# Performance work log

Hardware: AMD Instinct MI355X
Metric: run time of the kernel (lower is better)

## Reference

```python
import jax, jax.numpy as jnp
import numpy as np

B, N, C, H, W_, K, POS = 1, 100000, 128, 256, 256, 4, 36


def setup_inputs() -> dict:
    key = jax.random.key(0)
    ks = jax.random.split(key, 12)
    inp = {}
    # query coords in [-1, 1] (grid_sample normalized space)
    inp["query"] = jax.random.uniform(ks[0], (B, N, 3), jnp.float32, -1.0, 1.0)
    inp["pe"] = jax.random.normal(ks[1], (B, N, POS), jnp.float32)
    for i, p in enumerate(["xy", "xz", "yz"]):
        inp[f"feat_{p}"] = jax.random.normal(ks[2 + i], (B, C, H, W_), jnp.float32)
        inp[f"Wa_{p}"] = jax.random.normal(ks[5 + i], (POS, K), jnp.float32) * 0.1
        inp[f"ba_{p}"] = jnp.zeros((K,), jnp.float32)
        # offsets initialized to zero in the module; use small random so sampling is non-trivial
        inp[f"Wo_{p}"] = jax.random.normal(ks[8 + i], (POS, 2 * K), jnp.float32) * 0.02
        inp[f"bo_{p}"] = jnp.zeros((2 * K,), jnp.float32)
    return inp


def _bilinear_border(feat, gx, gy):
    """F.grid_sample(feat, grid, align_corners=False, padding_mode='border').
    feat: [B,C,H,W]; gx,gy: [B,N,K] normalized x (width) and y (height) coords.
    Returns [B,C,N,K]."""
    b, c, h, w = feat.shape
    # unnormalize (align_corners=False) then border-clip
    x = jnp.clip(((gx + 1.0) * w - 1.0) * 0.5, 0.0, w - 1.0)
    y = jnp.clip(((gy + 1.0) * h - 1.0) * 0.5, 0.0, h - 1.0)
    x0 = jnp.floor(x)
    y0 = jnp.floor(y)
    wx = x - x0  # [B,N,K]
    wy = y - y0
    xi0 = x0.astype(jnp.int32)
    yi0 = y0.astype(jnp.int32)
    xi1 = jnp.minimum(xi0 + 1, w - 1)
    yi1 = jnp.minimum(yi0 + 1, h - 1)
    ff = feat.reshape(b, c, h * w)
    gather = jax.vmap(lambda f, lin: f[:, lin])  # [C,HW],[N,K] -> [C,N,K]
    v00 = gather(ff, yi0 * w + xi0)
    v01 = gather(ff, yi0 * w + xi1)
    v10 = gather(ff, yi1 * w + xi0)
    v11 = gather(ff, yi1 * w + xi1)
    wx_ = wx[:, None]
    wy_ = wy[:, None]
    return (v00 * (1.0 - wx_) * (1.0 - wy_) + v01 * wx_ * (1.0 - wy_)
            + v10 * (1.0 - wx_) * wy_ + v11 * wx_ * wy_)


def _sample_plane(coords, pe, feat, Wa, ba, Wo, bo):
    b, n, _ = coords.shape
    attn = jax.nn.softmax(pe @ Wa + ba, axis=-1)            # [B,N,K]
    off = (pe @ Wo + bo).reshape(b, n, K, 2)                 # [B,N,K,2]
    sc = coords[:, :, None, :] + off                         # [B,N,K,2]
    # torch code flips last dim before grid_sample: grid x = sc[...,1], y = sc[...,0]
    sampled = _bilinear_border(feat, sc[..., 1], sc[..., 0])  # [B,C,N,K]
    out = jnp.einsum('bcnk,bnk->bnc', sampled, attn)         # weighted sum over K
    return out


def reference(query, pe, feat_xy, feat_xz, feat_yz,
              Wa_xy, ba_xy, Wo_xy, bo_xy,
              Wa_xz, ba_xz, Wo_xz, bo_xz,
              Wa_yz, ba_yz, Wo_yz, bo_yz):
    idx_xy = jnp.array([0, 1])
    idx_xz = jnp.array([0, 2])
    idx_yz = jnp.array([1, 2])
    f_xy = _sample_plane(query[..., idx_xy], pe, feat_xy, Wa_xy, ba_xy, Wo_xy, bo_xy)
    f_xz = _sample_plane(query[..., idx_xz], pe, feat_xz, Wa_xz, ba_xz, Wo_xz, bo_xz)
    f_yz = _sample_plane(query[..., idx_yz], pe, feat_yz, Wa_yz, ba_yz, Wo_yz, bo_yz)
    return f_xy + f_xz + f_yz
```

## Files before the change

### kernel.cpp

```cpp
#include <hip/hip_runtime.h>
#include <hip/hip_fp16.h>
#include <math.h>

#define NQ   100000
#define CCH  128
#define HDIM 256
#define WDIM 256
#define HW   (HDIM * WDIM)
#define KPTS 4
#define PDIM 36
#define NBIN 32768
#define RECW 40

#define WBLK ((NQ + 255) / 256)
#define TBLK ((HW / 64) * (CCH / 64) * 3)

__device__ inline int axis_bin(float x) {
  int b = (int)((x + 1.0f) * 16.0f);
  return min(31, max(0, b));
}
__device__ inline unsigned int spread5(unsigned int x) {
  return (x & 1u) | ((x & 2u) << 2) | ((x & 4u) << 4) | ((x & 8u) << 6) | ((x & 16u) << 8);
}
__device__ inline unsigned int bin_of(float x, float y, float z) {
  return spread5((unsigned int)axis_bin(x)) |
         (spread5((unsigned int)axis_bin(y)) << 1) |
         (spread5((unsigned int)axis_bin(z)) << 2);
}

__global__ void hist_kernel(const float* __restrict__ query,
                            unsigned int* __restrict__ counts) {
  const int q = blockIdx.x * 256 + threadIdx.x;
  if (q >= NQ) return;
  const unsigned int b = bin_of(query[q * 3 + 0], query[q * 3 + 1], query[q * 3 + 2]);
  atomicAdd(&counts[b], 1u);
}

__global__ void scan_kernel(const unsigned int* __restrict__ counts,
                            unsigned int* __restrict__ offs) {
  __shared__ unsigned int s[1024];
  const int t = threadIdx.x;
  unsigned int c[32];
  unsigned int sum = 0;
  const int base_i = t * 32;
#pragma unroll
  for (int j = 0; j < 32; ++j) { c[j] = counts[base_i + j]; sum += c[j]; }
  s[t] = sum;
  __syncthreads();
  for (int d = 1; d < 1024; d <<= 1) {
    const unsigned int v = (t >= d) ? s[t - d] : 0u;
    __syncthreads();
    s[t] += v;
    __syncthreads();
  }
  unsigned int run = s[t] - sum;
#pragma unroll
  for (int j = 0; j < 32; ++j) { offs[base_i + j] = run; run += c[j]; }
}

__global__ void fused_prep_kernel(const float* __restrict__ f0,
                                  const float* __restrict__ f1,
                                  const float* __restrict__ f2,
                                  __half2* __restrict__ featT,
                                  const float* __restrict__ query,
                                  const float* __restrict__ pe,
                                  unsigned int* __restrict__ offs,
                                  const float* __restrict__ Wa0, const float* __restrict__ ba0,
                                  const float* __restrict__ Wo0, const float* __restrict__ bo0,
                                  const float* __restrict__ Wa1, const float* __restrict__ ba1,
                                  const float* __restrict__ Wo1, const float* __restrict__ bo1,
                                  const float* __restrict__ Wa2, const float* __restrict__ ba2,
                                  const float* __restrict__ Wo2, const float* __restrict__ bo2,
                                  unsigned int* __restrict__ rec) {
  __shared__ float smem[64 * 65];
  const int bx = blockIdx.x;
  const int t = threadIdx.x;

  if (bx >= WBLK) {
    float (*tile)[65] = (float (*)[65])smem;
    const int tb = bx - WBLK;
    const int plane = tb >> 11;
    const int c64 = (tb >> 10) & 1;
    const int hw64 = tb & 1023;
    const float* __restrict__ f = (plane == 0) ? f0 : ((plane == 1) ? f1 : f2);
    __half2* __restrict__ o = featT + (size_t)plane * (size_t)HW * (CCH / 2);
    const int hw0 = hw64 * 64;
    const int c0 = c64 * 64;
    const int c_l = t >> 6;
    const int hw_l = t & 63;
#pragma unroll
    for (int i = 0; i < 16; ++i) {
      tile[c_l + 4 * i][hw_l] = f[(size_t)(c0 + c_l + 4 * i) * HW + (hw0 + hw_l)];
    }
    __syncthreads();
#pragma unroll
    for (int i = 0; i < 8; ++i) {
      const int idx = t + 256 * i;
      const int j = idx & 31;
      const int r = idx >> 5;
      o[(size_t)(hw0 + r) * (CCH / 2) + (c0 / 2 + j)] =
          __floats2half2_rn(tile[2 * j][r], tile[2 * j + 1][r]);
    }
    return;
  }

  float* sWa = smem;
  float* sWo = smem + 432;
  float* sba = smem + 1296;
  float* sbo = smem + 1308;
  {
    for (int i = t; i < 144; i += 256) { sWa[i] = Wa0[i]; sWa[144 + i] = Wa1[i]; sWa[288 + i] = Wa2[i]; }
    for (int i = t; i < 288; i += 256) { sWo[i] = Wo0[i]; sWo[288 + i] = Wo1[i]; sWo[576 + i] = Wo2[i]; }
    if (t < 4) { sba[0 + t] = ba0[t]; sba[4 + t] = ba1[t]; sba[8 + t] = ba2[t]; }
    if (t < 8) { sbo[0 + t] = bo0[t]; sbo[8 + t] = bo1[t]; sbo[16 + t] = bo2[t]; }
  }
  __syncthreads();

  const int q = bx * 256 + t;
  if (q >= NQ) return;

  float p[PDIM];
  const float4* pe4 = (const float4*)(pe + (size_t)q * PDIM);
#pragma unroll
  for (int i = 0; i < 9; ++i) {
    float4 v = pe4[i];
    p[4 * i + 0] = v.x; p[4 * i + 1] = v.y; p[4 * i + 2] = v.z; p[4 * i + 3] = v.w;
  }

  float la[3][4], of[3][8];
#pragma unroll
  for (int pl = 0; pl < 3; ++pl) {
#pragma unroll
    for (int k = 0; k < 4; ++k) la[pl][k] = sba[pl * 4 + k];
#pragma unroll
    for (int d = 0; d < 8; ++d) of[pl][d] = sbo[pl * 8 + d];
  }
#pragma unroll 4
  for (int j = 0; j < PDIM; ++j) {
    const float pj = p[j];
#pragma unroll
    for (int pl = 0; pl < 3; ++pl) {
#pragma unroll
      for (int k = 0; k < 4; ++k) la[pl][k] = fmaf(pj, sWa[(pl * PDIM + j) * 4 + k], la[pl][k]);
#pragma unroll
      for (int d = 0; d < 8; ++d) of[pl][d] = fmaf(pj, sWo[(pl * PDIM + j) * 8 + d], of[pl][d]);
    }
  }

  const float qx = query[q * 3 + 0];
  const float qy = query[q * 3 + 1];
  const float qz = query[q * 3 + 2];

  const unsigned int bin = bin_of(qx, qy, qz);
  const unsigned int pos = atomicAdd(&offs[bin], 1u);
  unsigned int* r = rec + (size_t)pos * RECW;
  r[0] = (unsigned int)q;

#pragma unroll
  for (int pl = 0; pl < 3; ++pl) {
    const float m = fmaxf(fmaxf(la[pl][0], la[pl][1]), fmaxf(la[pl][2], la[pl][3]));
    const float e0 = expf(la[pl][0] - m);
    const float e1 = expf(la[pl][1] - m);
    const float e2 = expf(la[pl][2] - m);
    const float e3 = expf(la[pl][3] - m);
    const float inv = 1.0f / (e0 + e1 + e2 + e3);
    float at[4] = {e0 * inv, e1 * inv, e2 * inv, e3 * inv};

    const float ca = (pl == 2) ? qy : qx;
    const float cb = (pl == 0) ? qy : qz;
    const unsigned int pbase = (unsigned int)pl * (unsigned int)HW * (CCH / 2);
#pragma unroll
    for (int k = 0; k < KPTS; ++k) {
      const float gy = ca + of[pl][k * 2 + 0];
      const float gx = cb + of[pl][k * 2 + 1];
      float x = ((gx + 1.0f) * (float)WDIM - 1.0f) * 0.5f;
      float y = ((gy + 1.0f) * (float)HDIM - 1.0f) * 0.5f;
      x = fminf(fmaxf(x, 0.0f), (float)(WDIM - 1));
      y = fminf(fmaxf(y, 0.0f), (float)(HDIM - 1));
      const float x0f = floorf(x), y0f = floorf(y);
      const float wx = x - x0f, wy = y - y0f;
      const int xi0 = (int)x0f, yi0 = (int)y0f;
      const unsigned int dx = (xi0 + 1 <= WDIM - 1) ? 1u : 0u;
      const unsigned int dy = (yi0 + 1 <= HDIM - 1) ? 1u : 0u;
      const float a = at[k];
      const float w00 = a * (1.0f - wx) * (1.0f - wy);
      const float w01 = a * wx * (1.0f - wy);
      const float w10 = a * (1.0f - wx) * wy;
      const float w11 = a * wx * wy;
      const unsigned int a00 = pbase + (unsigned int)(yi0 * WDIM + xi0) * (CCH / 2);
      const int j = pl * 4 + k;
      r[1 + 3 * j] = a00 | (dx << 24) | (dy << 25);
      const __half2 h01 = __floats2half2_rn(w00, w01);
      const __half2 h23 = __floats2half2_rn(w10, w11);
      r[2 + 3 * j] = *(const unsigned int*)&h01;
      r[3 + 3 * j] = *(const unsigned int*)&h23;
    }
  }
}

__global__ void sample_kernel(const unsigned int* __restrict__ rec,
                              const __half2* __restrict__ featT,
                              float* __restrict__ out) {
  const int lane = threadIdx.x & 63;
  const int wid = threadIdx.x >> 6;
  const int b = blockIdx.x;
  const int sb = (b & 7) * 3125 + (b >> 3);
  int i = sb * 4 + wid;
  i = __builtin_amdgcn_readfirstlane(i);

  const unsigned int* __restrict__ r = rec + (size_t)i * RECW;
  const int q = (int)r[0];

  unsigned int addr[12][4];
  unsigned int wu[12][2];
#pragma unroll
  for (int j = 0; j < 12; ++j) {
    const unsigned int pk = r[1 + 3 * j];
    wu[j][0] = r[2 + 3 * j];
    wu[j][1] = r[3 + 3 * j];
    const unsigned int a00 = pk & 0xFFFFFFu;
    const unsigned int xo = (pk >> 18) & 64u;
    const unsigned int yo = (pk >> 11) & 16384u;
    addr[j][0] = __builtin_amdgcn_readfirstlane(a00);
    addr[j][1] = __builtin_amdgcn_readfirstlane(a00 + xo);
    addr[j][2] = __builtin_amdgcn_readfirstlane(a00 + yo);
    addr[j][3] = __builtin_amdgcn_readfirstlane(a00 + xo + yo);
  }

  __half2 v[12][4];
#pragma unroll
  for (int j = 0; j < 12; ++j) {
#pragma unroll
    for (int c = 0; c < 4; ++c) {
      v[j][c] = *(featT + addr[j][c] + lane);
    }
  }

  float accx = 0.0f, accy = 0.0f;
#pragma unroll
  for (int j = 0; j < 12; ++j) {
    const __half2 h01 = __builtin_bit_cast(__half2, wu[j][0]);
    const __half2 h23 = __builtin_bit_cast(__half2, wu[j][1]);
    const float w00 = __low2float(h01);
    const float w01 = __high2float(h01);
    const float w10 = __low2float(h23);
    const float w11 = __high2float(h23);
    accx = fmaf(w00, __low2float(v[j][0]), accx);
    accy = fmaf(w00, __high2float(v[j][0]), accy);
    accx = fmaf(w01, __low2float(v[j][1]), accx);
    accy = fmaf(w01, __high2float(v[j][1]), accy);
    accx = fmaf(w10, __low2float(v[j][2]), accx);
    accy = fmaf(w10, __high2float(v[j][2]), accy);
    accx = fmaf(w11, __low2float(v[j][3]), accx);
    accy = fmaf(w11, __high2float(v[j][3]), accy);
  }
  *(float2*)(out + (size_t)q * CCH + lane * 2) = make_float2(accx, accy);
}

__global__ void fused_fallback(const float* __restrict__ query,
                               const float* __restrict__ pe,
                               const float* __restrict__ f0,
                               const float* __restrict__ f1,
                               const float* __restrict__ f2,
                               const float* __restrict__ Wa0, const float* __restrict__ ba0,
                               const float* __restrict__ Wo0, const float* __restrict__ bo0,
                               const float* __restrict__ Wa1, const float* __restrict__ ba1,
                               const float* __restrict__ Wo1, const float* __restrict__ bo1,
                               const float* __restrict__ Wa2, const float* __restrict__ ba2,
                               const float* __restrict__ Wo2, const float* __restrict__ bo2,
                               float* __restrict__ out) {
  const int lane = threadIdx.x & 63;
  const int wid = threadIdx.x >> 6;
  int q = blockIdx.x * 4 + wid;
  q = __builtin_amdgcn_readfirstlane(q);
  if (q >= NQ) return;
  const float qx = query[q * 3 + 0];
  const float qy = query[q * 3 + 1];
  const float qz = query[q * 3 + 2];
  const float* pep = pe + (size_t)q * PDIM;
  const int c0i = lane * 2, c1i = lane * 2 + 1;
  float accx = 0.0f, accy = 0.0f;
#pragma unroll
  for (int pl = 0; pl < 3; ++pl) {
    const float* Wa = (pl == 0) ? Wa0 : ((pl == 1) ? Wa1 : Wa2);
    const float* ba = (pl == 0) ? ba0 : ((pl == 1) ? ba1 : ba2);
    const float* Wo = (pl == 0) ? Wo0 : ((pl == 1) ? Wo1 : Wo2);
    const float* bo = (pl == 0) ? bo0 : ((pl == 1) ? bo1 : bo2);
    const float* f = (pl == 0) ? f0 : ((pl == 1) ? f1 : f2);
    float la[4] = {ba[0], ba[1], ba[2], ba[3]};
    float of[8];
    for (int d = 0; d < 8; ++d) of[d] = bo[d];
    for (int j = 0; j < PDIM; ++j) {
      const float pj = pep[j];
      for (int k = 0; k < 4; ++k) la[k] = fmaf(pj, Wa[j * 4 + k], la[k]);
      for (int d = 0; d < 8; ++d) of[d] = fmaf(pj, Wo[j * 8 + d], of[d]);
    }
    const float m = fmaxf(fmaxf(la[0], la[1]), fmaxf(la[2], la[3]));
    float e[4], s = 0.0f;
    for (int k = 0; k < 4; ++k) { e[k] = expf(la[k] - m); s += e[k]; }
    const float inv = 1.0f / s;
    const float ca = (pl == 2) ? qy : qx;
    const float cb = (pl == 0) ? qy : qz;
    for (int k = 0; k < 4; ++k) {
      const float gy = ca + of[k * 2 + 0];
      const float gx = cb + of[k * 2 + 1];
      float x = ((gx + 1.0f) * (float)WDIM - 1.0f) * 0.5f;
      float y = ((gy + 1.0f) * (float)HDIM - 1.0f) * 0.5f;
      x = fminf(fmaxf(x, 0.0f), (float)(WDIM - 1));
      y = fminf(fmaxf(y, 0.0f), (float)(HDIM - 1));
      const float x0f = floorf(x), y0f = floorf(y);
      const float wx = x - x0f, wy = y - y0f;
      const int xi0 = (int)x0f, yi0 = (int)y0f;
      const int xi1 = min(xi0 + 1, WDIM - 1);
      const int yi1 = min(yi0 + 1, HDIM - 1);
      const float a = e[k] * inv;
      const float w00 = a * (1.0f - wx) * (1.0f - wy);
      const float w01 = a * wx * (1.0f - wy);
      const float w10 = a * (1.0f - wx) * wy;
      const float w11 = a * wx * wy;
      const size_t p00 = (size_t)(yi0 * WDIM + xi0);
      const size_t p01 = (size_t)(yi0 * WDIM + xi1);
      const size_t p10 = (size_t)(yi1 * WDIM + xi0);
      const size_t p11 = (size_t)(yi1 * WDIM + xi1);
      const float* fa = f + (size_t)c0i * HW;
      const float* fb = f + (size_t)c1i * HW;
      accx += w00 * fa[p00] + w01 * fa[p01] + w10 * fa[p10] + w11 * fa[p11];
      accy += w00 * fb[p00] + w01 * fb[p01] + w10 * fb[p10] + w11 * fb[p11];
    }
  }
  *(float2*)(out + (size_t)q * CCH + lane * 2) = make_float2(accx, accy);
}

extern "C" void kernel_launch(void* const* d_in, const int* in_sizes, int n_in,
                              void* d_out, int out_size, void* d_ws, size_t ws_size,
                              hipStream_t stream) {
  const float* query = (const float*)d_in[0];
  const float* pe    = (const float*)d_in[1];
  const float* feat0 = (const float*)d_in[2];
  const float* Wa0   = (const float*)d_in[3];
  const float* ba0   = (const float*)d_in[4];
  const float* Wo0   = (const float*)d_in[5];
  const float* bo0   = (const float*)d_in[6];
  const float* feat1 = (const float*)d_in[7];
  const float* Wa1   = (const float*)d_in[8];
  const float* ba1   = (const float*)d_in[9];
  const float* Wo1   = (const float*)d_in[10];
  const float* bo1   = (const float*)d_in[11];
  const float* feat2 = (const float*)d_in[12];
  const float* Wa2   = (const float*)d_in[13];
  const float* ba2   = (const float*)d_in[14];
  const float* Wo2   = (const float*)d_in[15];
  const float* bo2   = (const float*)d_in[16];
  float* out = (float*)d_out;

  const size_t featT_elems = 3ull * HW * (CCH / 2);
  const size_t need = featT_elems * 4 + (size_t)NQ * RECW * 4 + (size_t)NBIN * 8;

  if (ws_size >= need) {
    __half2* featT = (__half2*)d_ws;
    unsigned int* rec = (unsigned int*)(d_ws) + featT_elems;
    unsigned int* counts = rec + (size_t)NQ * RECW;
    unsigned int* offs = counts + NBIN;

    hipMemsetAsync(counts, 0, NBIN * sizeof(unsigned int), stream);
    hist_kernel<<<dim3(WBLK), dim3(256), 0, stream>>>(query, counts);
    scan_kernel<<<dim3(1), dim3(1024), 0, stream>>>(counts, offs);
    fused_prep_kernel<<<dim3(WBLK + TBLK), dim3(256), 0, stream>>>(
        feat0, feat1, feat2, featT, query, pe, offs,
        Wa0, ba0, Wo0, bo0, Wa1, ba1, Wo1, bo1, Wa2, ba2, Wo2, bo2, rec);
    sample_kernel<<<dim3(NQ / 4), dim3(256), 0, stream>>>(rec, featT, out);
  } else {
    fused_fallback<<<dim3((NQ + 3) / 4), dim3(256), 0, stream>>>(
        query, pe, feat0, feat1, feat2,
        Wa0, ba0, Wo0, bo0, Wa1, ba1, Wo1, bo1, Wa2, ba2, Wo2, bo2, out);
  }
}
```

Baseline: 134.4 us.

## Use 16-byte gathers split across corner groups and coarsen spatial bins

The sample kernel now splits each wave into four 16-lane groups, one per bilinear corner. Each lane loads a 16-byte uint4 covering 8 channels instead of issuing four 4-byte loads, and the corner partial sums are combined with xor shuffles before 16 lanes write the output. Separately, the Morton binning used to sort queries is coarsened from 32 to 16 bins per axis (4096 bins), which makes the scan cheaper. This trades fewer, wider memory instructions for cross-lane reductions. The coarser bins may reduce locality in the sorted query order.

```diff
diff --git a/kernel.cpp b/kernel.cpp
--- a/kernel.cpp
+++ b/kernel.cpp
@@ -9,23 +9,23 @@
 #define HW   (HDIM * WDIM)
 #define KPTS 4
 #define PDIM 36
-#define NBIN 32768
+#define NBIN 4096
 #define RECW 40
 
 #define WBLK ((NQ + 255) / 256)
 #define TBLK ((HW / 64) * (CCH / 64) * 3)
 
 __device__ inline int axis_bin(float x) {
-  int b = (int)((x + 1.0f) * 16.0f);
-  return min(31, max(0, b));
-}
-__device__ inline unsigned int spread5(unsigned int x) {
-  return (x & 1u) | ((x & 2u) << 2) | ((x & 4u) << 4) | ((x & 8u) << 6) | ((x & 16u) << 8);
+  int b = (int)((x + 1.0f) * 8.0f);
+  return min(15, max(0, b));
+}
+__device__ inline unsigned int spread4(unsigned int x) {
+  return (x & 1u) | ((x & 2u) << 2) | ((x & 4u) << 4) | ((x & 8u) << 6);
 }
 __device__ inline unsigned int bin_of(float x, float y, float z) {
-  return spread5((unsigned int)axis_bin(x)) |
-         (spread5((unsigned int)axis_bin(y)) << 1) |
-         (spread5((unsigned int)axis_bin(z)) << 2);
+  return spread4((unsigned int)axis_bin(x)) |
+         (spread4((unsigned int)axis_bin(y)) << 1) |
+         (spread4((unsigned int)axis_bin(z)) << 2);
 }
 
 __global__ void hist_kernel(const float* __restrict__ query,
@@ -40,11 +40,11 @@
                             unsigned int* __restrict__ offs) {
   __shared__ unsigned int s[1024];
   const int t = threadIdx.x;
-  unsigned int c[32];
-  unsigned int sum = 0;
-  const int base_i = t * 32;
-#pragma unroll
-  for (int j = 0; j < 32; ++j) { c[j] = counts[base_i + j]; sum += c[j]; }
+  const unsigned int c0 = counts[4 * t + 0];
+  const unsigned int c1 = counts[4 * t + 1];
+  const unsigned int c2 = counts[4 * t + 2];
+  const unsigned int c3 = counts[4 * t + 3];
+  const unsigned int sum = c0 + c1 + c2 + c3;
   s[t] = sum;
   __syncthreads();
   for (int d = 1; d < 1024; d <<= 1) {
@@ -53,9 +53,11 @@
     s[t] += v;
     __syncthreads();
   }
-  unsigned int run = s[t] - sum;
-#pragma unroll
-  for (int j = 0; j < 32; ++j) { offs[base_i + j] = run; run += c[j]; }
+  const unsigned int base = s[t] - sum;
+  offs[4 * t + 0] = base;
+  offs[4 * t + 1] = base + c0;
+  offs[4 * t + 2] = base + c0 + c1;
+  offs[4 * t + 3] = base + c0 + c1 + c2;
 }
 
 __global__ void fused_prep_kernel(const float* __restrict__ f0,
@@ -211,50 +213,61 @@
   const unsigned int* __restrict__ r = rec + (size_t)i * RECW;
   const int q = (int)r[0];
 
-  unsigned int addr[12][4];
-  unsigned int wu[12][2];
+  const int g = lane >> 4;
+  const unsigned int l4 = (lane & 15) * 4;
+  const unsigned int m1 = (g & 1) ? 0xFFFFFFFFu : 0u;
+  const unsigned int m2 = (g & 2) ? 0xFFFFFFFFu : 0u;
+
+  unsigned int addr[12];
+  float w[12];
 #pragma unroll
   for (int j = 0; j < 12; ++j) {
-    const unsigned int pk = r[1 + 3 * j];
-    wu[j][0] = r[2 + 3 * j];
-    wu[j][1] = r[3 + 3 * j];
+    const unsigned int pk = __builtin_amdgcn_readfirstlane(r[1 + 3 * j]);
+    const unsigned int w01u = __builtin_amdgcn_readfirstlane(r[2 + 3 * j]);
+    const unsigned int w23u = __builtin_amdgcn_readfirstlane(r[3 + 3 * j]);
     const unsigned int a00 = pk & 0xFFFFFFu;
     const unsigned int xo = (pk >> 18) & 64u;
     const unsigned int yo = (pk >> 11) & 16384u;
-    addr[j][0] = __builtin_amdgcn_readfirstlane(a00);
-    addr[j][1] = __builtin_amdgcn_readfirstlane(a00 + xo);
-    addr[j][2] = __builtin_amdgcn_readfirstlane(a00 + yo);
-    addr[j][3] = __builtin_amdgcn_readfirstlane(a00 + xo + yo);
-  }
-
-  __half2 v[12][4];
+    addr[j] = a00 + (xo & m1) + (yo & m2) + l4;
+    const unsigned int hv = m2 ? w23u : w01u;
+    const unsigned int hw = m1 ? (hv >> 16) : (hv & 0xFFFFu);
+    w[j] = __low2float(__builtin_bit_cast(__half2, hw));
+  }
+
+  uint4 v[12];
 #pragma unroll
   for (int j = 0; j < 12; ++j) {
-#pragma unroll
-    for (int c = 0; c < 4; ++c) {
-      v[j][c] = *(featT + addr[j][c] + lane);
-    }
-  }
-
-  float accx = 0.0f, accy = 0.0f;
+    v[j] = *(const uint4*)(featT + addr[j]);
+  }
+
+  float acc[8] = {0.f, 0.f, 0.f, 0.f, 0.f, 0.f, 0.f, 0.f};
 #pragma unroll
   for (int j = 0; j < 12; ++j) {
-    const __half2 h01 = __builtin_bit_cast(__half2, wu[j][0]);
-    const __half2 h23 = __builtin_bit_cast(__half2, wu[j][1]);
-    const float w00 = __low2float(h01);
-    const float w01 = __high2float(h01);
-    const float w10 = __low2float(h23);
-    const float w11 = __high2float(h23);
-    accx = fmaf(w00, __low2float(v[j][0]), accx);
-    accy = fmaf(w00, __high2float(v[j][0]), accy);
-    accx = fmaf(w01, __low2float(v[j][1]), accx);
-    accy = fmaf(w01, __high2float(v[j][1]), accy);
-    accx = fmaf(w10, __low2float(v[j][2]), accx);
-    accy = fmaf(w10, __high2float(v[j][2]), accy);
-    accx = fmaf(w11, __low2float(v[j][3]), accx);
-    accy = fmaf(w11, __high2float(v[j][3]), accy);
-  }
-  *(float2*)(out + (size_t)q * CCH + lane * 2) = make_float2(accx, accy);
+    const __half2 h0 = __builtin_bit_cast(__half2, v[j].x);
+    const __half2 h1 = __builtin_bit_cast(__half2, v[j].y);
+    const __half2 h2 = __builtin_bit_cast(__half2, v[j].z);
+    const __half2 h3 = __builtin_bit_cast(__half2, v[j].w);
+    const float wj = w[j];
+    acc[0] = fmaf(wj, __low2float(h0), acc[0]);
+    acc[1] = fmaf(wj, __high2float(h0), acc[1]);
+    acc[2] = fmaf(wj, __low2float(h1), acc[2]);
+    acc[3] = fmaf(wj, __high2float(h1), acc[3]);
+    acc[4] = fmaf(wj, __low2float(h2), acc[4]);
+    acc[5] = fmaf(wj, __high2float(h2), acc[5]);
+    acc[6] = fmaf(wj, __low2float(h3), acc[6]);
+    acc[7] = fmaf(wj, __high2float(h3), acc[7]);
+  }
+
+#pragma unroll
+  for (int c = 0; c < 8; ++c) acc[c] += __shfl_xor(acc[c], 32, 64);
+#pragma unroll
+  for (int c = 0; c < 8; ++c) acc[c] += __shfl_xor(acc[c], 16, 64);
+
+  if (lane < 16) {
+    float* op = out + (size_t)q * CCH + lane * 8;
+    *(float4*)op = make_float4(acc[0], acc[1], acc[2], acc[3]);
+    *(float4*)(op + 4) = make_float4(acc[4], acc[5], acc[6], acc[7]);
+  }
 }
 
 __global__ void fused_fallback(const float* __restrict__ query,
```

New measurement: 130.3 us. 3.0% less time.
